# Performance work log

Hardware: AMD Instinct MI355X
Metric: run time of the kernel (lower is better)

Reference implementation:

```python
import jax, jax.numpy as jnp
import numpy as np

N_NODES = 100000
N_EDGES = 50000
NNZ = 1600000
C = 128
EPS = 0.0  # train_eps=False -> fixed buffer


def setup_inputs() -> dict:
    key = jax.random.key(0)
    k0, k1, k2, k3, k4 = jax.random.split(key, 5)
    x_0 = jax.random.normal(k0, (N_NODES, C), dtype=jnp.float32)
    node_idx = jax.random.randint(k1, (NNZ,), 0, N_NODES, dtype=jnp.int64)
    edge_idx = jax.random.randint(k2, (NNZ,), 0, N_EDGES, dtype=jnp.int64)
    # Linear(in_channels, in_channels) params (kaiming-uniform-ish scale)
    lim = 1.0 / np.sqrt(C)
    W = jax.random.uniform(k3, (C, C), minval=-lim, maxval=lim, dtype=jnp.float32)
    b = jax.random.uniform(k4, (C,), minval=-lim, maxval=lim, dtype=jnp.float32)
    return {"x_0": x_0, "node_idx": node_idx, "edge_idx": edge_idx, "W": W, "b": b}


def reference(x_0, node_idx, edge_idx, W, b):
    # Step 1: x_1 = B_1^T @ x_0  (hyperedge e sums features of its nodes)
    x_1 = jax.ops.segment_sum(x_0[node_idx], edge_idx, num_segments=N_EDGES)
    # Step 2: m_{1->0} = B_1 @ x_1 (node sums features of its incident hyperedges)
    m_1_0 = jax.ops.segment_sum(x_1[edge_idx], node_idx, num_segments=N_NODES)
    # Step 3: GIN update: Theta @ ((1+eps)*x_0 + m)
    out_0 = ((1.0 + EPS) * x_0 + m_1_0) @ W.T + b
    return (out_0, x_1)
```

## Files before the change

### kernel.cpp

```cpp
#include <hip/hip_runtime.h>
#include <stdint.h>

#define N_NODES 100000
#define N_EDGES 50000
#define C 128
#define NB 196
#define CAP 12288
#define X0_BLOCKS 25000
#define WBLOCKS 32
#define PCHUNK 8192

typedef short short8 __attribute__((ext_vector_type(8)));
typedef float f32x4  __attribute__((ext_vector_type(4)));

__device__ __forceinline__ unsigned int bf16rne(float f) {
    unsigned int u = __float_as_uint(f);
    return (u + 0x7FFFu + ((u >> 16) & 1u)) >> 16;
}
__device__ __forceinline__ unsigned int pk_bf16(float x, float y) {
    return (bf16rne(y) << 16) | bf16rne(x);
}
__device__ __forceinline__ float bf_lo(unsigned int u) { return __uint_as_float(u << 16); }
__device__ __forceinline__ float bf_hi(unsigned int u) { return __uint_as_float(u & 0xFFFF0000u); }

__global__ __launch_bounds__(256) void conv_hist(
    const float2* __restrict__ x0, const float2* __restrict__ W,
    unsigned int* __restrict__ x0h, unsigned int* __restrict__ Whu,
    const int* __restrict__ nidx, const int* __restrict__ eidx,
    int* __restrict__ Ceh, int* __restrict__ Cnh, int nnz)
{
    __shared__ int he[NB], hn[NB];
    int bid = blockIdx.x, t = threadIdx.x;
    if (bid < X0_BLOCKS) {
        int i = bid * 256 + t;
        float2 v = x0[i];
        x0h[i] = pk_bf16(v.x, v.y);
        return;
    }
    if (bid < X0_BLOCKS + WBLOCKS) {
        int i = (bid - X0_BLOCKS) * 256 + t;
        float2 v = W[i];
        Whu[i] = pk_bf16(v.x, v.y);
        return;
    }
    int chunk0 = (bid - X0_BLOCKS - WBLOCKS) * PCHUNK;
    for (int k = t; k < NB; k += 256) { he[k] = 0; hn[k] = 0; }
    __syncthreads();
#pragma unroll 4
    for (int j = 0; j < PCHUNK / 256; ++j) {
        int i = chunk0 + j * 256 + t;
        if (i < nnz) {
            atomicAdd(&he[eidx[i] >> 8], 1);
            atomicAdd(&hn[nidx[i] >> 9], 1);
        }
    }
    __syncthreads();
    for (int k = t; k < NB; k += 256) {
        if (he[k]) atomicAdd(&Ceh[k], he[k]);
        if (hn[k]) atomicAdd(&Cnh[k], hn[k]);
    }
}

__global__ __launch_bounds__(256) void coarse_scan(
    const int* __restrict__ Ceh, const int* __restrict__ Cnh,
    int* __restrict__ Cecur, int* __restrict__ Cncur)
{
    __shared__ int s[256];
    int t = threadIdx.x;
    int v = (t < NB) ? Ceh[t] : 0;
    s[t] = v; __syncthreads();
    for (int d = 1; d < 256; d <<= 1) {
        int u = (t >= d) ? s[t - d] : 0;
        __syncthreads(); s[t] += u; __syncthreads();
    }
    if (t < NB) Cecur[t] = s[t] - v;
    __syncthreads();
    v = (t < NB) ? Cnh[t] : 0;
    s[t] = v; __syncthreads();
    for (int d = 1; d < 256; d <<= 1) {
        int u = (t >= d) ? s[t - d] : 0;
        __syncthreads(); s[t] += u; __syncthreads();
    }
    if (t < NB) Cncur[t] = s[t] - v;
}

__global__ __launch_bounds__(256) void partition_kernel(
    const int* __restrict__ nidx, const int* __restrict__ eidx,
    int* __restrict__ Cecur, int* __restrict__ Cncur,
    unsigned int* __restrict__ pe, unsigned int* __restrict__ pn, int nnz)
{
    __shared__ int he[NB], hn[NB], be[NB], bn[NB];
    int t = threadIdx.x;
    int chunk0 = blockIdx.x * PCHUNK;
    for (int k = t; k < NB; k += 256) { he[k] = 0; hn[k] = 0; }
    __syncthreads();
#pragma unroll 4
    for (int j = 0; j < PCHUNK / 256; ++j) {
        int i = chunk0 + j * 256 + t;
        if (i < nnz) {
            atomicAdd(&he[eidx[i] >> 8], 1);
            atomicAdd(&hn[nidx[i] >> 9], 1);
        }
    }
    __syncthreads();
    for (int k = t; k < NB; k += 256) {
        be[k] = atomicAdd(&Cecur[k], he[k]);
        bn[k] = atomicAdd(&Cncur[k], hn[k]);
        he[k] = 0; hn[k] = 0;
    }
    __syncthreads();
#pragma unroll 4
    for (int j = 0; j < PCHUNK / 256; ++j) {
        int i = chunk0 + j * 256 + t;
        if (i < nnz) {
            int e = eidx[i], n = nidx[i];
            int re = atomicAdd(&he[e >> 8], 1);
            pe[be[e >> 8] + re] = (unsigned int)((e & 255) | (n << 8));
            int rn = atomicAdd(&hn[n >> 9], 1);
            pn[bn[n >> 9] + rn] = (unsigned int)((n & 511) | (e << 9));
        }
    }
}

__global__ __launch_bounds__(256) void bucket_scatter_ex(
    const unsigned int* __restrict__ pe, const unsigned int* __restrict__ pn,
    const int* __restrict__ Cecur, const int* __restrict__ Cncur,
    int* __restrict__ e_list, int* __restrict__ n_list,
    int* __restrict__ eoff, int* __restrict__ noff)
{
    __shared__ int cnt[512], cur[512], s[256];
    __shared__ int vals[CAP];
    bool eside = blockIdx.x < NB;
    int b = eside ? blockIdx.x : blockIdx.x - NB;
    const unsigned int* pairs = eside ? pe : pn;
    const int* endarr         = eside ? Cecur : Cncur;
    int* out                  = eside ? e_list : n_list;
    int* off                  = eside ? eoff : noff;
    int shift = eside ? 8 : 9;
    int mask  = (1 << shift) - 1;
    int kpb   = 1 << shift;
    int nkeys = eside ? N_EDGES : N_NODES;
    int key0 = b * kpb;
    int nk = nkeys - key0; if (nk > kpb) nk = kpb;
    if (nk <= 0) return;
    int start = (b == 0) ? 0 : endarr[b - 1];
    int end   = endarr[b];
    int t = threadIdx.x;

    for (int k = t; k < nk; k += 256) cnt[k] = 0;
    __syncthreads();
    for (int i = start + t; i < end; i += 256)
        atomicAdd(&cnt[(int)(pairs[i] & mask)], 1);
    __syncthreads();
    int k0 = 2 * t, k1 = 2 * t + 1;
    int c0 = (k0 < nk) ? cnt[k0] : 0;
    int c1 = (k1 < nk) ? cnt[k1] : 0;
    int local = c0 + c1;
    s[t] = local; __syncthreads();
    for (int d = 1; d < 256; d <<= 1) {
        int u = (t >= d) ? s[t - d] : 0;
        __syncthreads(); s[t] += u; __syncthreads();
    }
    int excl = s[t] - local;
    if (k0 < nk) { cur[k0] = excl;      off[key0 + k0] = start + excl; }
    if (k1 < nk) { cur[k1] = excl + c0; off[key0 + k1] = start + excl + c0; }
    if (b == NB - 1 && t == 0) off[nkeys] = end;
    __syncthreads();
    for (int i = start + t; i < end; i += 256) {
        unsigned int p = pairs[i];
        int key = (int)(p & mask);
        int val = (int)(p >> shift);
        int pos = atomicAdd(&cur[key], 1);
        if (pos < CAP) vals[pos] = val;
        else out[start + pos] = val;
    }
    __syncthreads();
    int sz = end - start; if (sz > CAP) sz = CAP;
    for (int j = t; j < sz; j += 256) out[start + j] = vals[j];
}

__device__ __forceinline__ float2 gather_bf16_rows(
    const unsigned int* __restrict__ src, const int* __restrict__ list,
    int s0, int s1, int lane)
{
    float ax0=0,ay0=0,ax1=0,ay1=0,ax2=0,ay2=0,ax3=0,ay3=0;
    float ax4=0,ay4=0,ax5=0,ay5=0,ax6=0,ay6=0,ax7=0,ay7=0;
    for (int base = s0; base < s1; base += 64) {
        int cnt = s1 - base; if (cnt > 64) cnt = 64;
        int my = (lane < cnt) ? list[base + lane] : 0;
        int j = 0;
        for (; j + 8 <= cnt; j += 8) {
            int g0 = __shfl(my, j+0), g1 = __shfl(my, j+1);
            int g2 = __shfl(my, j+2), g3 = __shfl(my, j+3);
            int g4 = __shfl(my, j+4), g5 = __shfl(my, j+5);
            int g6 = __shfl(my, j+6), g7 = __shfl(my, j+7);
            unsigned int u0 = src[(size_t)g0 * 64 + lane];
            unsigned int u1 = src[(size_t)g1 * 64 + lane];
            unsigned int u2 = src[(size_t)g2 * 64 + lane];
            unsigned int u3 = src[(size_t)g3 * 64 + lane];
            unsigned int u4 = src[(size_t)g4 * 64 + lane];
            unsigned int u5 = src[(size_t)g5 * 64 + lane];
            unsigned int u6 = src[(size_t)g6 * 64 + lane];
            unsigned int u7 = src[(size_t)g7 * 64 + lane];
            ax0 += bf_lo(u0); ay0 += bf_hi(u0);  ax1 += bf_lo(u1); ay1 += bf_hi(u1);
            ax2 += bf_lo(u2); ay2 += bf_hi(u2);  ax3 += bf_lo(u3); ay3 += bf_hi(u3);
            ax4 += bf_lo(u4); ay4 += bf_hi(u4);  ax5 += bf_lo(u5); ay5 += bf_hi(u5);
            ax6 += bf_lo(u6); ay6 += bf_hi(u6);  ax7 += bf_lo(u7); ay7 += bf_hi(u7);
        }
        for (; j < cnt; ++j) {
            int g = __shfl(my, j);
            unsigned int u = src[(size_t)g * 64 + lane];
            ax0 += bf_lo(u); ay0 += bf_hi(u);
        }
    }
    ax0+=ax1; ay0+=ay1; ax2+=ax3; ay2+=ay3; ax4+=ax5; ay4+=ay5; ax6+=ax7; ay6+=ay7;
    ax0+=ax2; ay0+=ay2; ax4+=ax6; ay4+=ay6;
    ax0+=ax4; ay0+=ay4;
    return make_float2(ax0, ay0);
}

__global__ __launch_bounds__(256) void seg_sum(
    const unsigned int* __restrict__ x0h, const int* __restrict__ list,
    const int* __restrict__ off, float2* __restrict__ x1,
    unsigned int* __restrict__ x1h, int nseg)
{
    int wid  = (blockIdx.x * 256 + threadIdx.x) >> 6;
    int lane = threadIdx.x & 63;
    if (wid >= nseg) return;
    float2 acc = gather_bf16_rows(x0h, list, off[wid], off[wid + 1], lane);
    x1 [(size_t)wid * 64 + lane] = acc;
    x1h[(size_t)wid * 64 + lane] = pk_bf16(acc.x, acc.y);
}

__global__ __launch_bounds__(256) void m_gather(
    unsigned int* __restrict__ x0h, const unsigned int* __restrict__ x1h,
    const int* __restrict__ n_list, const int* __restrict__ noff)
{
    int wid  = (blockIdx.x * 256 + threadIdx.x) >> 6;
    int lane = threadIdx.x & 63;
    if (wid >= N_NODES) return;
    unsigned int bu = x0h[(size_t)wid * 64 + lane];
    float2 g = gather_bf16_rows(x1h, n_list, noff[wid], noff[wid + 1], lane);
    g.x += bf_lo(bu); g.y += bf_hi(bu);
    x0h[(size_t)wid * 64 + lane] = pk_bf16(g.x, g.y);
}

__global__ __launch_bounds__(256) void gin_gemm_mfma(
    const unsigned int* __restrict__ mh,
    const unsigned short* __restrict__ Wh, const float* __restrict__ b,
    float* __restrict__ out)
{
    int t = threadIdx.x;
    int lane = t & 63, w = t >> 6;
    int wrow0 = blockIdx.x * 64 + w * 16;
    if (wrow0 >= N_NODES) return;
    int l15  = lane & 15;
    int koff = (lane >> 4) * 8;
    const unsigned short* mrow = (const unsigned short*)mh + (size_t)(wrow0 + l15) * C;

    f32x4 acc[8];
#pragma unroll
    for (int n = 0; n < 8; ++n) acc[n] = (f32x4){0, 0, 0, 0};
#pragma unroll
    for (int kt = 0; kt < C; kt += 32) {
        short8 a = *(const short8*)&mrow[kt + koff];
#pragma unroll
        for (int n = 0; n < 8; ++n) {
            short8 bb = *(const short8*)&Wh[(size_t)(n * 16 + l15) * C + kt + koff];
            acc[n] = __builtin_amdgcn_mfma_f32_16x16x32_bf16(a, bb, acc[n], 0, 0, 0);
        }
    }
    int drow = wrow0 + (lane >> 4) * 4;
#pragma unroll
    for (int n = 0; n < 8; ++n) {
        int colg = n * 16 + l15;
        float bias = b[colg];
#pragma unroll
        for (int j = 0; j < 4; ++j)
            out[(size_t)(drow + j) * C + colg] = acc[n][j] + bias;
    }
}

__global__ __launch_bounds__(256) void scatter_rows(
    const float4* __restrict__ src, const int* __restrict__ gather_idx,
    const int* __restrict__ scatter_idx, float* __restrict__ dst, int nnz)
{
    int gid = blockIdx.x * 256 + threadIdx.x;
    int row = gid >> 5, lane = gid & 31;
    if (row >= nnz) return;
    float4 v = src[(size_t)gather_idx[row] * 32 + lane];
    float* d = dst + (size_t)scatter_idx[row] * C + lane * 4;
    atomicAdd(d + 0, v.x); atomicAdd(d + 1, v.y);
    atomicAdd(d + 2, v.z); atomicAdd(d + 3, v.w);
}

__global__ __launch_bounds__(256) void gin_gemm(
    const float* __restrict__ x0, const float* __restrict__ m,
    const float* __restrict__ W, const float* __restrict__ b,
    float* __restrict__ out)
{
    __shared__ float Ws[32][129];
    __shared__ float insf[32][33];
    int t = threadIdx.x;
    int col = t & 127, rg = t >> 7;
    int row0 = blockIdx.x * 32;
    float acc[16];
#pragma unroll
    for (int r = 0; r < 16; ++r) acc[r] = 0.f;
    float bias = b[col];
    for (int kt = 0; kt < C; kt += 32) {
#pragma unroll
        for (int j = 0; j < 16; ++j) {
            int i = j * 256 + t, wc = i >> 5, kl = i & 31;
            Ws[kl][wc] = W[(size_t)wc * C + kt + kl];
        }
#pragma unroll
        for (int j = 0; j < 4; ++j) {
            int i = j * 256 + t, r = i >> 5, kl = i & 31;
            size_t gi = (size_t)(row0 + r) * C + kt + kl;
            insf[r][kl] = x0[gi] + m[gi];
        }
        __syncthreads();
#pragma unroll
        for (int kl = 0; kl < 32; ++kl) {
            float wv = Ws[kl][col];
#pragma unroll
            for (int r = 0; r < 16; ++r)
                acc[r] += insf[rg * 16 + r][kl] * wv;
        }
        __syncthreads();
    }
#pragma unroll
    for (int r = 0; r < 16; ++r)
        out[(size_t)(row0 + rg * 16 + r) * C + col] = acc[r] + bias;
}

extern "C" void kernel_launch(void* const* d_in, const int* in_sizes, int n_in,
                              void* d_out, int out_size, void* d_ws, size_t ws_size,
                              hipStream_t stream) {
    const float* x0 = (const float*)d_in[0];
    const int* nidx = (const int*)d_in[1];
    const int* eidx = (const int*)d_in[2];
    const float* W  = (const float*)d_in[3];
    const float* b  = (const float*)d_in[4];

    float* out0 = (float*)d_out;
    float* x1   = out0 + (size_t)N_NODES * C;
    int nnz = in_sizes[1];

    auto align256 = [](char* q) {
        return (char*)(((uintptr_t)q + 255) & ~(uintptr_t)255);
    };
    char* p = align256((char*)d_ws);
    unsigned int* pe = (unsigned int*)p; p = align256(p + (size_t)nnz * 4);
    unsigned int* pn = (unsigned int*)p; p = align256(p + (size_t)nnz * 4);
    unsigned int* x0h = (unsigned int*)p; p = align256(p + (size_t)N_NODES * 64 * 4);
    unsigned int* x1h = (unsigned int*)p; p = align256(p + (size_t)N_EDGES * 64 * 4);
    int* e_list = (int*)p; p = align256(p + (size_t)nnz * 4);
    int* n_list = (int*)p; p = align256(p + (size_t)nnz * 4);
    int* eoff   = (int*)p; p = align256(p + (size_t)(N_EDGES + 1) * 4);
    int* noff   = (int*)p; p = align256(p + (size_t)(N_NODES + 1) * 4);
    int* Ceh    = (int*)p;
    int* Cnh    = Ceh + NB;
    p = align256((char*)(Cnh + NB));
    int* Cecur  = (int*)p; p = align256(p + NB * 4);
    int* Cncur  = (int*)p; p = align256(p + NB * 4);
    unsigned int* Whu = (unsigned int*)p; p = align256(p + (size_t)C * C / 2 * 4);
    size_t needed = (size_t)(p - (char*)d_ws);

    if (ws_size < needed) {
        float* m = (float*)d_ws;
        hipMemsetAsync(x1, 0, (size_t)N_EDGES * C * sizeof(float), stream);
        hipMemsetAsync(m,  0, (size_t)N_NODES * C * sizeof(float), stream);
        int blocks = (nnz + 7) / 8;
        scatter_rows<<<blocks, 256, 0, stream>>>((const float4*)x0, nidx, eidx, x1, nnz);
        scatter_rows<<<blocks, 256, 0, stream>>>((const float4*)x1, eidx, nidx, m, nnz);
        gin_gemm<<<N_NODES / 32, 256, 0, stream>>>(x0, m, W, b, out0);
        return;
    }

    int pblocks = (nnz + PCHUNK - 1) / PCHUNK;

    hipMemsetAsync(Ceh, 0, 2 * NB * sizeof(int), stream);
    conv_hist<<<X0_BLOCKS + WBLOCKS + pblocks, 256, 0, stream>>>(
        (const float2*)x0, (const float2*)W, x0h, Whu, nidx, eidx, Ceh, Cnh, nnz);

    coarse_scan<<<1, 256, 0, stream>>>(Ceh, Cnh, Cecur, Cncur);
    partition_kernel<<<pblocks, 256, 0, stream>>>(
        nidx, eidx, Cecur, Cncur, pe, pn, nnz);
    bucket_scatter_ex<<<2 * NB, 256, 0, stream>>>(
        pe, pn, Cecur, Cncur, e_list, n_list, eoff, noff);

    seg_sum<<<(N_EDGES * 64 + 255) / 256, 256, 0, stream>>>(
        x0h, e_list, eoff, (float2*)x1, x1h, N_EDGES);

    m_gather<<<(N_NODES * 64 + 255) / 256, 256, 0, stream>>>(
        x0h, x1h, n_list, noff);

    gin_gemm_mfma<<<(N_NODES + 63) / 64, 256, 0, stream>>>(
        x0h, (const unsigned short*)Whu, b, out0);
}
```

Before: 245.4 us.

## Fuse node gather into MFMA GEMM via shared-memory staging

```diff
diff --git a/kernel.cpp b/kernel.cpp
--- a/kernel.cpp
+++ b/kernel.cpp
@@ -232,38 +232,38 @@
     x1h[(size_t)wid * 64 + lane] = pk_bf16(acc.x, acc.y);
 }
 
-__global__ __launch_bounds__(256) void m_gather(
-    unsigned int* __restrict__ x0h, const unsigned int* __restrict__ x1h,
-    const int* __restrict__ n_list, const int* __restrict__ noff)
-{
-    int wid  = (blockIdx.x * 256 + threadIdx.x) >> 6;
-    int lane = threadIdx.x & 63;
-    if (wid >= N_NODES) return;
-    unsigned int bu = x0h[(size_t)wid * 64 + lane];
-    float2 g = gather_bf16_rows(x1h, n_list, noff[wid], noff[wid + 1], lane);
-    g.x += bf_lo(bu); g.y += bf_hi(bu);
-    x0h[(size_t)wid * 64 + lane] = pk_bf16(g.x, g.y);
-}
-
-__global__ __launch_bounds__(256) void gin_gemm_mfma(
-    const unsigned int* __restrict__ mh,
+__global__ __launch_bounds__(256) void gin_fused2(
+    const unsigned int* __restrict__ x0h, const unsigned int* __restrict__ x1h,
+    const int* __restrict__ n_list, const int* __restrict__ noff,
     const unsigned short* __restrict__ Wh, const float* __restrict__ b,
     float* __restrict__ out)
 {
+    __shared__ __align__(16) unsigned short ins[64][136];
     int t = threadIdx.x;
     int lane = t & 63, w = t >> 6;
     int wrow0 = blockIdx.x * 64 + w * 16;
-    if (wrow0 >= N_NODES) return;
+
+    for (int r = 0; r < 16; ++r) {
+        int node = wrow0 + r;
+        float2 g = make_float2(0.f, 0.f);
+        if (node < N_NODES) {
+            unsigned int bu = x0h[(size_t)node * 64 + lane];
+            g = gather_bf16_rows(x1h, n_list, noff[node], noff[node + 1], lane);
+            g.x += bf_lo(bu); g.y += bf_hi(bu);
+        }
+        *(unsigned int*)&ins[w * 16 + r][lane * 2] = pk_bf16(g.x, g.y);
+    }
+
     int l15  = lane & 15;
     int koff = (lane >> 4) * 8;
-    const unsigned short* mrow = (const unsigned short*)mh + (size_t)(wrow0 + l15) * C;
+    int arow = w * 16 + l15;
 
     f32x4 acc[8];
 #pragma unroll
     for (int n = 0; n < 8; ++n) acc[n] = (f32x4){0, 0, 0, 0};
 #pragma unroll
     for (int kt = 0; kt < C; kt += 32) {
-        short8 a = *(const short8*)&mrow[kt + koff];
+        short8 a = *(const short8*)&ins[arow][kt + koff];
 #pragma unroll
         for (int n = 0; n < 8; ++n) {
             short8 bb = *(const short8*)&Wh[(size_t)(n * 16 + l15) * C + kt + koff];
@@ -277,7 +277,8 @@
         float bias = b[colg];
 #pragma unroll
         for (int j = 0; j < 4; ++j)
-            out[(size_t)(drow + j) * C + colg] = acc[n][j] + bias;
+            if (drow + j < N_NODES)
+                out[(size_t)(drow + j) * C + colg] = acc[n][j] + bias;
     }
 }
 
@@ -394,9 +395,6 @@
     seg_sum<<<(N_EDGES * 64 + 255) / 256, 256, 0, stream>>>(
         x0h, e_list, eoff, (float2*)x1, x1h, N_EDGES);
 
-    m_gather<<<(N_NODES * 64 + 255) / 256, 256, 0, stream>>>(
-        x0h, x1h, n_list, noff);
-
-    gin_gemm_mfma<<<(N_NODES + 63) / 64, 256, 0, stream>>>(
-        x0h, (const unsigned short*)Whu, b, out0);
-}
+    gin_fused2<<<(N_NODES + 63) / 64, 256, 0, stream>>>(
+        x0h, x1h, n_list, noff, (const unsigned short*)Whu, b, out0);
+}
```

New measurement: 279.0 us. 13.7% more time.
